# Kernel tuning notes

Hardware: AMD Instinct MI355X
Metric: run time of the kernel (lower is better)

Reference implementation:

```python
import jax, jax.numpy as jnp
import numpy as np

B, S, D, H = 4, 2048, 512, 8
DH = D // H


def setup_inputs() -> dict:
    key = jax.random.key(0)
    ks = jax.random.split(key, 7)
    scale = 1.0 / np.sqrt(DH)  # mimic nn.Linear init magnitude
    return {
        "x": jax.random.normal(ks[0], (B, S, D), dtype=jnp.float32),
        "Wq": jax.random.normal(ks[1], (H, DH, DH), dtype=jnp.float32) * scale,
        "bq": jax.random.normal(ks[2], (H, DH), dtype=jnp.float32) * scale,
        "Wk": jax.random.normal(ks[3], (H, DH, DH), dtype=jnp.float32) * scale,
        "bk": jax.random.normal(ks[4], (H, DH), dtype=jnp.float32) * scale,
        "Wv": jax.random.normal(ks[5], (H, DH, DH), dtype=jnp.float32) * scale,
        "bv": jax.random.normal(ks[6], (H, DH), dtype=jnp.float32) * scale,
    }


def reference(x, Wq, bq, Wk, bk, Wv, bv):
    # x: [B, S, D] -> per-head slices [B, S, H, DH] (contiguous chunks, as in torch slicing)
    xh = x.reshape(B, S, H, DH)
    # nn.Linear: y = x @ W.T + b, per head. Wq[h] is [out, in].
    q = jnp.einsum("bshd,hed->bshe", xh, Wq) + bq  # [B, S, H, DH]
    k = jnp.einsum("bshd,hed->bshe", xh, Wk) + bk
    v = jnp.einsum("bshd,hed->bshe", xh, Wv) + bv
    scores = jnp.einsum("bshe,bthe->bhst", q, k) / jnp.sqrt(jnp.float32(DH))  # [B, H, S, S]
    attn = jax.nn.softmax(scores, axis=-1)
    out = jnp.einsum("bhst,bthe->bshe", attn, v)  # [B, S, H, DH]
    return out.reshape(B, S, D)  # hstack of head outputs == concat along feature dim
```

## Files before the change

### kernel.cpp

```cpp
#include <hip/hip_runtime.h>
#include <math.h>

#define B_ 4
#define S_ 2048
#define D_ 512
#define H_ 8
#define DH_ 64
#define BH_ (B_*H_)
#define SCALE 0.1803368801111243f

typedef __attribute__((ext_vector_type(4)))  float f32x4;
typedef __attribute__((ext_vector_type(16))) float f32x16;
typedef __attribute__((ext_vector_type(8)))  short bf16x8;
typedef __attribute__((ext_vector_type(4)))  uint  u32x4;

__device__ inline uint rnepk(float a, float b) {
    uint ua = __builtin_bit_cast(uint, a), ub = __builtin_bit_cast(uint, b);
    ua += 0x7FFFu + ((ua >> 16) & 1u);
    ub += 0x7FFFu + ((ub >> 16) & 1u);
    return (ua >> 16) | (ub & 0xFFFF0000u);
}
__device__ inline uint truncpk(float lo, float hi) {
    return __builtin_amdgcn_perm(__builtin_bit_cast(uint, hi),
                                 __builtin_bit_cast(uint, lo), 0x07060302u);
}
__device__ inline f32x16 zero16() {
    f32x16 z;
    #pragma unroll
    for (int i = 0; i < 16; ++i) z[i] = 0.f;
    return z;
}
__device__ inline bf16x8 pack8(f32x4 a, f32x4 c) {
    u32x4 u;
    u.x = rnepk(a[0], a[1]); u.y = rnepk(a[2], a[3]);
    u.z = rnepk(c[0], c[1]); u.w = rnepk(c[2], c[3]);
    return __builtin_bit_cast(bf16x8, u);
}

#if __has_builtin(__builtin_amdgcn_permlane32_swap)
__device__ inline void lane32swap(uint& a, uint& b) {
    typedef __attribute__((ext_vector_type(2))) uint u32x2;
    u32x2 r = __builtin_amdgcn_permlane32_swap(a, b, false, false);
    a = r.x; b = r.y;
}
#else
__device__ inline void lane32swap(uint& a, uint& b) {
    const int l5 = (threadIdx.x & 63) >> 5;
    uint send = l5 ? a : b;
    uint recv = __shfl_xor(send, 32);
    uint an = l5 ? recv : a;
    uint bn = l5 ? b : recv;
    a = an; b = bn;
}
#endif

__device__ inline void dma16(const ushort* g, ushort* l) {
    __builtin_amdgcn_global_load_lds(
        (const __attribute__((address_space(1))) unsigned int*)g,
        (__attribute__((address_space(3))) unsigned int*)l, 16, 0, 0);
}

__global__ __launch_bounds__(256)
void prep_w(const float* __restrict__ Wq, const float* __restrict__ Wk,
            const float* __restrict__ Wv, ushort* __restrict__ Wf)
{
    const int pb = blockIdx.x;
    const int proj = pb >> 3, h = pb & 7;
    const float* W = (proj == 0 ? Wq : proj == 1 ? Wk : Wv) + h * DH_ * DH_;
    #pragma unroll
    for (int it = 0; it < 2; ++it) {
        const int slot = threadIdx.x + it * 256;
        const int c = slot >> 6, lane = slot & 63;
        const int l31 = lane & 31, l5 = lane >> 5;
        const int et = c >> 2, st = c & 3;
        const float* wr = W + (et * 32 + l31) * DH_ + st * 16 + l5 * 8;
        bf16x8 v = pack8(*(const f32x4*)wr, *(const f32x4*)(wr + 4));
        *(bf16x8*)(Wf + ((size_t)pb * 8 + c) * 512 + lane * 8) = v;
    }
}

__global__ __launch_bounds__(256, 2)
void qkv_mfma(const float* __restrict__ x,
              const float* __restrict__ bq, const float* __restrict__ bk,
              const float* __restrict__ bv, const ushort* __restrict__ Wf,
              ushort* __restrict__ Qf, ushort* __restrict__ Kf,
              ushort* __restrict__ Vf)
{
    const int bh = blockIdx.x, b = bh >> 3, h = bh & 7;
    const int sblk = blockIdx.y, s0 = sblk * 128;
    const int tid = threadIdx.x;
    const int w = tid >> 6, lane = tid & 63, l31 = lane & 31, l5 = lane >> 5;

    __shared__ __align__(16) ushort bnc[4][2560];
    __shared__ __align__(16) ushort vsh[64 * 136];
    ushort* mybnc = bnc[w];

    const ushort* wqb = Wf + ((size_t)(0 * 8 + h)) * 8 * 512;
    const ushort* wkb = Wf + ((size_t)(1 * 8 + h)) * 8 * 512;
    const ushort* wvb = Wf + ((size_t)(2 * 8 + h)) * 8 * 512;

    const int srow = w * 32 + l31;
    const float* xr = x + ((size_t)(b * S_ + s0 + srow)) * D_ + h * DH_;
    bf16x8 xf[4];
    #pragma unroll
    for (int st = 0; st < 4; ++st)
        xf[st] = pack8(*(const f32x4*)(xr + st * 16 + l5 * 8),
                       *(const f32x4*)(xr + st * 16 + l5 * 8 + 4));

    {
        bf16x8 wf[2][4];
        #pragma unroll
        for (int et = 0; et < 2; ++et)
            #pragma unroll
            for (int st = 0; st < 4; ++st)
                wf[et][st] = *(const bf16x8*)(wkb + (et * 4 + st) * 512 + lane * 8);
        #pragma unroll
        for (int et = 0; et < 2; ++et) {
            f32x16 acc = zero16();
            #pragma unroll
            for (int st = 0; st < 4; ++st)
                acc = __builtin_amdgcn_mfma_f32_32x32x16_bf16(wf[et][st], xf[st], acc, 0, 0, 0);
            #pragma unroll
            for (int rg = 0; rg < 4; ++rg) {
                float4 b4 = *(const float4*)(bk + h * DH_ + et * 32 + rg * 8 + l5 * 4);
                uint2 pk;
                pk.x = rnepk(acc[rg * 4 + 0] + b4.x, acc[rg * 4 + 1] + b4.y);
                pk.y = rnepk(acc[rg * 4 + 2] + b4.z, acc[rg * 4 + 3] + b4.w);
                *(uint2*)(mybnc + l31 * 72 + et * 32 + rg * 8 + l5 * 4) = pk;
            }
        }
        const int kt = sblk * 2 + (w >> 1), g = w & 1;
        ushort* kd = Kf + (((size_t)(bh * 32 + kt)) * 2 + g) * 2048;
        #pragma unroll
        for (int st = 0; st < 4; ++st) {
            uint4 v = *(const uint4*)(mybnc + l31 * 72 + st * 16 + l5 * 8);
            *(uint4*)(kd + st * 512 + lane * 8) = v;
        }
    }

    {
        bf16x8 wf[2][4];
        #pragma unroll
        for (int et = 0; et < 2; ++et)
            #pragma unroll
            for (int st = 0; st < 4; ++st)
                wf[et][st] = *(const bf16x8*)(wqb + (et * 4 + st) * 512 + lane * 8);
        #pragma unroll
        for (int et = 0; et < 2; ++et) {
            f32x16 acc = zero16();
            #pragma unroll
            for (int st = 0; st < 4; ++st)
                acc = __builtin_amdgcn_mfma_f32_32x32x16_bf16(wf[et][st], xf[st], acc, 0, 0, 0);
            #pragma unroll
            for (int rg = 0; rg < 4; ++rg) {
                float4 b4 = *(const float4*)(bq + h * DH_ + et * 32 + rg * 8 + l5 * 4);
                uint2 pk;
                pk.x = rnepk((acc[rg * 4 + 0] + b4.x) * SCALE, (acc[rg * 4 + 1] + b4.y) * SCALE);
                pk.y = rnepk((acc[rg * 4 + 2] + b4.z) * SCALE, (acc[rg * 4 + 3] + b4.w) * SCALE);
                *(uint2*)(mybnc + l31 * 72 + et * 32 + rg * 8 + l5 * 4) = pk;
            }
        }
        ushort* qd = Qf + ((size_t)(bh * 64 + sblk * 4 + w)) * 2048;
        #pragma unroll
        for (int st = 0; st < 4; ++st) {
            uint4 v = *(const uint4*)(mybnc + l31 * 72 + st * 16 + l5 * 8);
            *(uint4*)(qd + st * 512 + lane * 8) = v;
        }
    }

    {
        bf16x8 wf[2][4];
        #pragma unroll
        for (int et = 0; et < 2; ++et)
            #pragma unroll
            for (int st = 0; st < 4; ++st)
                wf[et][st] = *(const bf16x8*)(wvb + (et * 4 + st) * 512 + lane * 8);
        #pragma unroll
        for (int et = 0; et < 2; ++et) {
            f32x16 acc = zero16();
            #pragma unroll
            for (int st = 0; st < 4; ++st)
                acc = __builtin_amdgcn_mfma_f32_32x32x16_bf16(xf[st], wf[et][st], acc, 0, 0, 0);
            const float bb = bv[h * DH_ + et * 32 + l31];
            #pragma unroll
            for (int rg = 0; rg < 4; ++rg) {
                uint2 pk;
                pk.x = rnepk(acc[rg * 4 + 0] + bb, acc[rg * 4 + 1] + bb);
                pk.y = rnepk(acc[rg * 4 + 2] + bb, acc[rg * 4 + 3] + bb);
                *(uint2*)(vsh + (et * 32 + l31) * 136 + w * 32 + rg * 8 + l5 * 4) = pk;
            }
        }
        __syncthreads();
        #pragma unroll
        for (int i = 0; i < 4; ++i) {
            const int c = w * 4 + i;
            const int ktl = c >> 3, dht = (c >> 2) & 1, st = c & 3;
            uint4 v = *(const uint4*)(vsh + (dht * 32 + l31) * 136 + ktl * 64 + st * 16 + l5 * 8);
            *(uint4*)(Vf + (((size_t)(bh * 32 + sblk * 2 + ktl)) * 2 + dht) * 2048
                      + st * 512 + lane * 8) = v;
        }
    }
}

__global__ __launch_bounds__(512, 4)
void flash_mfma(const ushort* __restrict__ Qf, const ushort* __restrict__ Kf,
                const ushort* __restrict__ Vf, float* __restrict__ out)
{
    const int bh = blockIdx.x, qblk = blockIdx.y;
    const int b = bh >> 3, h = bh & 7;
    const int tid = threadIdx.x;
    const int w = tid >> 6, lane = tid & 63, l31 = lane & 31, l5 = lane >> 5;
    const int qi = w & 3, p = w >> 2;

    __shared__ __align__(16) ushort lds_u[32768];

    const ushort* gsrc = (((w >> 1) & 1) ? Vf : Kf)
                         + (size_t)bh * 32 * 4096 + (size_t)(w & 1) * 2048;
    const int stp = w >> 2;
    ushort* const stdst0 = lds_u + w * 2048;

    {
        const ushort* gb = gsrc + (size_t)stp * 4096;
        #pragma unroll
        for (int i = 0; i < 4; ++i)
            dma16(gb + i * 512 + lane * 8, stdst0 + i * 512);
    }

    bf16x8 qf[4];
    #pragma unroll
    for (int st = 0; st < 4; ++st)
        qf[st] = *(const bf16x8*)(Qf + ((size_t)(bh * 64 + qblk * 4 + qi)) * 2048
                                  + st * 512 + lane * 8);

    f32x16 O[2];
    O[0] = zero16(); O[1] = zero16();
    float lsum = 0.f;

    for (int step = 0; step < 16; ++step) {
        __syncthreads();
        const ushort* cbuf = lds_u + (step & 1) * 16384;
        if (step < 15) {
            const ushort* gb = gsrc + (size_t)(2 * (step + 1) + stp) * 4096;
            ushort* ld = lds_u + ((step + 1) & 1) * 16384 + w * 2048;
            #pragma unroll
            for (int i = 0; i < 4; ++i)
                dma16(gb + i * 512 + lane * 8, ld + i * 512);
        }
        const ushort* kreg = cbuf + p * 8192;
        const ushort* vreg = kreg + 4096;

        bf16x8 pf[4];
        #pragma unroll
        for (int g = 0; g < 2; ++g) {
            bf16x8 kf[4];
            #pragma unroll
            for (int st = 0; st < 4; ++st)
                kf[st] = *(const bf16x8*)(kreg + (g * 4 + st) * 512 + lane * 8);
            f32x16 sc_ = zero16();
            __builtin_amdgcn_s_setprio(1);
            #pragma unroll
            for (int st = 0; st < 4; ++st)
                sc_ = __builtin_amdgcn_mfma_f32_32x32x16_bf16(kf[st], qf[st], sc_, 0, 0, 0);
            __builtin_amdgcn_s_setprio(0);
            uint pr[8];
            #pragma unroll
            for (int rg = 0; rg < 4; ++rg) {
                float p0 = __builtin_amdgcn_exp2f(sc_[rg * 4 + 0]);
                float p1 = __builtin_amdgcn_exp2f(sc_[rg * 4 + 1]);
                float p2 = __builtin_amdgcn_exp2f(sc_[rg * 4 + 2]);
                float p3 = __builtin_amdgcn_exp2f(sc_[rg * 4 + 3]);
                lsum += (p0 + p1) + (p2 + p3);
                pr[2 * rg + 0] = truncpk(p0, p1);
                pr[2 * rg + 1] = truncpk(p2, p3);
            }
            #pragma unroll
            for (int pp = 0; pp < 2; ++pp) {
                lane32swap(pr[4 * pp + 0], pr[4 * pp + 2]);
                lane32swap(pr[4 * pp + 1], pr[4 * pp + 3]);
                u32x4 u; u.x = pr[4 * pp + 0]; u.y = pr[4 * pp + 1];
                u.z = pr[4 * pp + 2]; u.w = pr[4 * pp + 3];
                pf[g * 2 + pp] = __builtin_bit_cast(bf16x8, u);
            }
        }

        #pragma unroll
        for (int dht = 0; dht < 2; ++dht) {
            bf16x8 vf[4];
            #pragma unroll
            for (int st = 0; st < 4; ++st)
                vf[st] = *(const bf16x8*)(vreg + (dht * 4 + st) * 512 + lane * 8);
            __builtin_amdgcn_s_setprio(1);
            #pragma unroll
            for (int st = 0; st < 4; ++st)
                O[dht] = __builtin_amdgcn_mfma_f32_32x32x16_bf16(vf[st], pf[st], O[dht], 0, 0, 0);
            __builtin_amdgcn_s_setprio(0);
        }
    }

    lsum += __shfl_xor(lsum, 32);

    __syncthreads();
    float* mb = (float*)lds_u;
    float* reg = mb + qi * 2176;
    float* lsA = mb + 4 * 2176;

    if (p == 1) {
        #pragma unroll
        for (int dht = 0; dht < 2; ++dht)
            #pragma unroll
            for (int rg = 0; rg < 4; ++rg) {
                f32x4 v4;
                v4[0] = O[dht][rg * 4 + 0];
                v4[1] = O[dht][rg * 4 + 1];
                v4[2] = O[dht][rg * 4 + 2];
                v4[3] = O[dht][rg * 4 + 3];
                *(f32x4*)(reg + l31 * 68 + dht * 32 + rg * 8 + l5 * 4) = v4;
            }
        if (l5 == 0) lsA[qi * 32 + l31] = lsum;
    }
    __syncthreads();
    if (p == 0) {
        const float linv = 1.0f / (lsum + lsA[qi * 32 + l31]);
        #pragma unroll
        for (int dht = 0; dht < 2; ++dht)
            #pragma unroll
            for (int rg = 0; rg < 4; ++rg) {
                float* a = reg + l31 * 68 + dht * 32 + rg * 8 + l5 * 4;
                f32x4 part = *(const f32x4*)a;
                f32x4 v4;
                v4[0] = (O[dht][rg * 4 + 0] + part[0]) * linv;
                v4[1] = (O[dht][rg * 4 + 1] + part[1]) * linv;
                v4[2] = (O[dht][rg * 4 + 2] + part[2]) * linv;
                v4[3] = (O[dht][rg * 4 + 3] + part[3]) * linv;
                *(f32x4*)a = v4;
            }
    }
    __syncthreads();

    const int q0 = qblk * 128;
    #pragma unroll
    for (int i = 0; i < 4; ++i) {
        const int slot = tid + 512 * i;
        const int r = slot >> 4, c = slot & 15;
        f32x4 v = *(const f32x4*)(mb + (r >> 5) * 2176 + (r & 31) * 68 + c * 4);
        *(f32x4*)(out + ((size_t)(b * S_ + q0 + r)) * D_ + h * DH_ + c * 4) = v;
    }
}

extern "C" void kernel_launch(void* const* d_in, const int* in_sizes, int n_in,
                              void* d_out, int out_size, void* d_ws, size_t ws_size,
                              hipStream_t stream) {
    const float* x  = (const float*)d_in[0];
    const float* Wq = (const float*)d_in[1];
    const float* bq = (const float*)d_in[2];
    const float* Wk = (const float*)d_in[3];
    const float* bk = (const float*)d_in[4];
    const float* Wv = (const float*)d_in[5];
    const float* bv = (const float*)d_in[6];
    float* outp = (float*)d_out;

    ushort* Qf  = (ushort*)d_ws;
    ushort* Kf  = Qf + (size_t)BH_ * S_ * DH_;
    ushort* Vf  = Kf + (size_t)BH_ * S_ * DH_;
    ushort* Wfb = Vf + (size_t)BH_ * S_ * DH_;

    prep_w<<<dim3(24), 256, 0, stream>>>(Wq, Wk, Wv, Wfb);
    qkv_mfma<<<dim3(BH_, S_ / 128), 256, 0, stream>>>(x, bq, bk, bv, Wfb,
                                                      Qf, Kf, Vf);
    flash_mfma<<<dim3(BH_, 16), 512, 0, stream>>>(Qf, Kf, Vf, outp);
}
```

Before: 126.0 us.

## Interleave softmax exp with QK and PV MFMAs in attention inner loop

New measurement: 126.0 us. No clear change (+0.0%).

```diff
diff --git a/kernel.cpp b/kernel.cpp
--- a/kernel.cpp
+++ b/kernel.cpp
@@ -59,6 +59,25 @@
         (const __attribute__((address_space(1))) unsigned int*)g,
         (__attribute__((address_space(3))) unsigned int*)l, 16, 0, 0);
 }
+
+#define SMQ(SC, RG) do {                                                     \
+    float p0_ = __builtin_amdgcn_exp2f(SC[RG * 4 + 0]);                      \
+    float p1_ = __builtin_amdgcn_exp2f(SC[RG * 4 + 1]);                      \
+    float p2_ = __builtin_amdgcn_exp2f(SC[RG * 4 + 2]);                      \
+    float p3_ = __builtin_amdgcn_exp2f(SC[RG * 4 + 3]);                      \
+    lsum += (p0_ + p1_) + (p2_ + p3_);                                       \
+    pr[2 * RG + 0] = truncpk(p0_, p1_);                                      \
+    pr[2 * RG + 1] = truncpk(p2_, p3_);                                      \
+} while (0)
+
+#define SWAPPF(PF0, PF1) do {                                                \
+    lane32swap(pr[0], pr[2]); lane32swap(pr[1], pr[3]);                      \
+    lane32swap(pr[4], pr[6]); lane32swap(pr[5], pr[7]);                      \
+    u32x4 u0_; u0_.x = pr[0]; u0_.y = pr[1]; u0_.z = pr[2]; u0_.w = pr[3];   \
+    u32x4 u1_; u1_.x = pr[4]; u1_.y = pr[5]; u1_.z = pr[6]; u1_.w = pr[7];   \
+    PF0 = __builtin_bit_cast(bf16x8, u0_);                                   \
+    PF1 = __builtin_bit_cast(bf16x8, u1_);                                   \
+} while (0)
 
 __global__ __launch_bounds__(256)
 void prep_w(const float* __restrict__ Wq, const float* __restrict__ Wk,
@@ -232,8 +251,9 @@
         qf[st] = *(const bf16x8*)(Qf + ((size_t)(bh * 64 + qblk * 4 + qi)) * 2048
                                   + st * 512 + lane * 8);
 
+    const f32x16 fz = zero16();
     f32x16 O[2];
-    O[0] = zero16(); O[1] = zero16();
+    O[0] = fz; O[1] = fz;
     float lsum = 0.f;
 
     for (int step = 0; step < 16; ++step) {
@@ -249,52 +269,60 @@
         const ushort* kreg = cbuf + p * 8192;
         const ushort* vreg = kreg + 4096;
 
-        bf16x8 pf[4];
-        #pragma unroll
-        for (int g = 0; g < 2; ++g) {
-            bf16x8 kf[4];
-            #pragma unroll
-            for (int st = 0; st < 4; ++st)
-                kf[st] = *(const bf16x8*)(kreg + (g * 4 + st) * 512 + lane * 8);
-            f32x16 sc_ = zero16();
-            __builtin_amdgcn_s_setprio(1);
-            #pragma unroll
-            for (int st = 0; st < 4; ++st)
-                sc_ = __builtin_amdgcn_mfma_f32_32x32x16_bf16(kf[st], qf[st], sc_, 0, 0, 0);
-            __builtin_amdgcn_s_setprio(0);
-            uint pr[8];
-            #pragma unroll
-            for (int rg = 0; rg < 4; ++rg) {
-                float p0 = __builtin_amdgcn_exp2f(sc_[rg * 4 + 0]);
-                float p1 = __builtin_amdgcn_exp2f(sc_[rg * 4 + 1]);
-                float p2 = __builtin_amdgcn_exp2f(sc_[rg * 4 + 2]);
-                float p3 = __builtin_amdgcn_exp2f(sc_[rg * 4 + 3]);
-                lsum += (p0 + p1) + (p2 + p3);
-                pr[2 * rg + 0] = truncpk(p0, p1);
-                pr[2 * rg + 1] = truncpk(p2, p3);
-            }
-            #pragma unroll
-            for (int pp = 0; pp < 2; ++pp) {
-                lane32swap(pr[4 * pp + 0], pr[4 * pp + 2]);
-                lane32swap(pr[4 * pp + 1], pr[4 * pp + 3]);
-                u32x4 u; u.x = pr[4 * pp + 0]; u.y = pr[4 * pp + 1];
-                u.z = pr[4 * pp + 2]; u.w = pr[4 * pp + 3];
-                pf[g * 2 + pp] = __builtin_bit_cast(bf16x8, u);
-            }
-        }
-
-        #pragma unroll
-        for (int dht = 0; dht < 2; ++dht) {
-            bf16x8 vf[4];
-            #pragma unroll
-            for (int st = 0; st < 4; ++st)
-                vf[st] = *(const bf16x8*)(vreg + (dht * 4 + st) * 512 + lane * 8);
-            __builtin_amdgcn_s_setprio(1);
-            #pragma unroll
-            for (int st = 0; st < 4; ++st)
-                O[dht] = __builtin_amdgcn_mfma_f32_32x32x16_bf16(vf[st], pf[st], O[dht], 0, 0, 0);
-            __builtin_amdgcn_s_setprio(0);
-        }
+        bf16x8 k0 = *(const bf16x8*)(kreg + 0 * 512 + lane * 8);
+        bf16x8 k1 = *(const bf16x8*)(kreg + 1 * 512 + lane * 8);
+        bf16x8 k2 = *(const bf16x8*)(kreg + 2 * 512 + lane * 8);
+        bf16x8 k3 = *(const bf16x8*)(kreg + 3 * 512 + lane * 8);
+        __builtin_amdgcn_s_setprio(1);
+        f32x16 sc0 = __builtin_amdgcn_mfma_f32_32x32x16_bf16(k0, qf[0], fz,  0, 0, 0);
+        sc0        = __builtin_amdgcn_mfma_f32_32x32x16_bf16(k1, qf[1], sc0, 0, 0, 0);
+        sc0        = __builtin_amdgcn_mfma_f32_32x32x16_bf16(k2, qf[2], sc0, 0, 0, 0);
+        sc0        = __builtin_amdgcn_mfma_f32_32x32x16_bf16(k3, qf[3], sc0, 0, 0, 0);
+        __builtin_amdgcn_s_setprio(0);
+
+        bf16x8 g0 = *(const bf16x8*)(kreg + 4 * 512 + lane * 8);
+        bf16x8 g1 = *(const bf16x8*)(kreg + 5 * 512 + lane * 8);
+        bf16x8 g2 = *(const bf16x8*)(kreg + 6 * 512 + lane * 8);
+        bf16x8 g3 = *(const bf16x8*)(kreg + 7 * 512 + lane * 8);
+        bf16x8 va0 = *(const bf16x8*)(vreg + 0 * 512 + lane * 8);
+        bf16x8 va1 = *(const bf16x8*)(vreg + 1 * 512 + lane * 8);
+        bf16x8 vb0 = *(const bf16x8*)(vreg + 4 * 512 + lane * 8);
+        bf16x8 vb1 = *(const bf16x8*)(vreg + 5 * 512 + lane * 8);
+
+        uint pr[8];
+        f32x16 sc1 = __builtin_amdgcn_mfma_f32_32x32x16_bf16(g0, qf[0], fz,  0, 0, 0);
+        SMQ(sc0, 0);
+        sc1        = __builtin_amdgcn_mfma_f32_32x32x16_bf16(g1, qf[1], sc1, 0, 0, 0);
+        SMQ(sc0, 1);
+        sc1        = __builtin_amdgcn_mfma_f32_32x32x16_bf16(g2, qf[2], sc1, 0, 0, 0);
+        SMQ(sc0, 2);
+        sc1        = __builtin_amdgcn_mfma_f32_32x32x16_bf16(g3, qf[3], sc1, 0, 0, 0);
+        SMQ(sc0, 3);
+        bf16x8 pf0, pf1;
+        SWAPPF(pf0, pf1);
+
+        O[0] = __builtin_amdgcn_mfma_f32_32x32x16_bf16(va0, pf0, O[0], 0, 0, 0);
+        SMQ(sc1, 0);
+        O[0] = __builtin_amdgcn_mfma_f32_32x32x16_bf16(va1, pf1, O[0], 0, 0, 0);
+        SMQ(sc1, 1);
+        O[1] = __builtin_amdgcn_mfma_f32_32x32x16_bf16(vb0, pf0, O[1], 0, 0, 0);
+        SMQ(sc1, 2);
+        O[1] = __builtin_amdgcn_mfma_f32_32x32x16_bf16(vb1, pf1, O[1], 0, 0, 0);
+        SMQ(sc1, 3);
+        bf16x8 pf2, pf3;
+        SWAPPF(pf2, pf3);
+
+        bf16x8 va2 = *(const bf16x8*)(vreg + 2 * 512 + lane * 8);
+        bf16x8 va3 = *(const bf16x8*)(vreg + 3 * 512 + lane * 8);
+        bf16x8 vb2 = *(const bf16x8*)(vreg + 6 * 512 + lane * 8);
+        bf16x8 vb3 = *(const bf16x8*)(vreg + 7 * 512 + lane * 8);
+
+        __builtin_amdgcn_s_setprio(1);
+        O[0] = __builtin_amdgcn_mfma_f32_32x32x16_bf16(va2, pf2, O[0], 0, 0, 0);
+        O[0] = __builtin_amdgcn_mfma_f32_32x32x16_bf16(va3, pf3, O[0], 0, 0, 0);
+        O[1] = __builtin_amdgcn_mfma_f32_32x32x16_bf16(vb2, pf2, O[1], 0, 0, 0);
+        O[1] = __builtin_amdgcn_mfma_f32_32x32x16_bf16(vb3, pf3, O[1], 0, 0, 0);
+        __builtin_amdgcn_s_setprio(0);
     }
 
     lsum += __shfl_xor(lsum, 32);
```
